# Optimization experiments

Hardware: AMD Instinct MI355X
Metric: run time of the kernel (lower is better)

The kernel has to match this reference:

```python
import jax, jax.numpy as jnp
import numpy as np

B, S, HID = 1, 2048, 2048
H, KVH, D = 16, 8, 128
QR, KR, VR = 6, 2, 2
SOFTCAP = 50.0
SCALING = D ** -0.5
NEG = -1e9


def _rope(Bfac, cos, sin):
    # Bfac: [b, s, r, d]; cos/sin: [s, d//2]; rotates adjacent pairs (complex view)
    x = Bfac.reshape(*Bfac.shape[:-1], D // 2, 2)
    xe, xo = x[..., 0], x[..., 1]
    c = cos[None, :, None, :]
    s = sin[None, :, None, :]
    oe = xe * c - xo * s
    oo = xe * s + xo * c
    return jnp.stack([oe, oo], axis=-1).reshape(Bfac.shape)


def setup_inputs() -> dict:
    key = jax.random.key(0)
    ks = jax.random.split(key, 12)
    hidden_states = jax.random.normal(ks[0], (B, S, HID), jnp.float32)
    # rotary tables (standard RoPE frequencies)
    inv_freq = 1.0 / (10000.0 ** (jnp.arange(0, D, 2, dtype=jnp.float32) / D))
    t = jnp.arange(S, dtype=jnp.float32)
    ang = t[:, None] * inv_freq[None, :]            # [S, D//2]
    cos, sin = jnp.cos(ang), jnp.sin(ang)
    # causal additive mask [1,1,S,S]
    causal = jnp.tril(jnp.ones((S, S), bool))
    mask = jnp.where(causal, 0.0, NEG).astype(jnp.float32)[None, None]
    kv_write_indices = jnp.arange(S, dtype=jnp.int32)
    sc = lambda k, shp: jax.random.normal(k, shp, jnp.float32) * (shp[0] ** -0.5)
    return {
        "hidden_states": hidden_states, "cos": cos, "sin": sin, "mask": mask,
        "kv_write_indices": kv_write_indices,
        "WAq": sc(ks[1], (HID, H * QR)), "WAk": sc(ks[2], (HID, KVH * KR)),
        "WAv": sc(ks[3], (HID, KVH * VR)), "WBq": sc(ks[4], (HID, QR * D)),
        "WBk": sc(ks[5], (HID, KR * D)), "WBv": sc(ks[6], (HID, VR * D)),
        "Wo": sc(ks[7], (H * D, HID)),
    }


def reference(hidden_states, cos, sin, mask, kv_write_indices,
              WAq, WAk, WAv, WBq, WBk, WBv, Wo):
    b, s, _ = hidden_states.shape
    # factor projections (never materialize full Q/K/V)
    A_q = (hidden_states @ WAq).reshape(b, s, H, QR)
    A_k = (hidden_states @ WAk).reshape(b, s, KVH, KR)
    A_v = (hidden_states @ WAv).reshape(b, s, KVH, VR)
    B_q = (hidden_states @ WBq).reshape(b, s, QR, D)
    B_k = (hidden_states @ WBk).reshape(b, s, KR, D)
    B_v = (hidden_states @ WBv).reshape(b, s, VR, D)
    # RoPE on B factors
    B_q = _rope(B_q, cos, sin)
    B_k = _rope(B_k, cos, sin)
    # prefill: kv_write_indices = arange(S) => cache slices equal current factors
    # GQA: broadcast KV heads up to H
    hpk = H // KVH
    A_k = jnp.repeat(A_k, hpk, axis=2)   # [b,k,H,KR]
    A_v = jnp.repeat(A_v, hpk, axis=2)   # [b,k,H,VR]
    # factor-expanded attention scores
    B_dots = jnp.einsum('bqrd,bksd->bqkrs', B_q, B_k) * SCALING
    attn = jnp.einsum('bqhr,bkhs,bqkrs->bhqk', A_q, A_k, B_dots)
    # logit softcapping
    attn = SOFTCAP * jnp.tanh(attn / SOFTCAP)
    attn = attn + mask
    probs = jax.nn.softmax(attn.astype(jnp.float32), axis=-1).astype(hidden_states.dtype)
    # factor-expanded output
    out = jnp.einsum('bhqk,bkhu,bkud->bhqd', probs, A_v, B_v)
    out = out.transpose(0, 2, 1, 3).reshape(b, s, H * D)
    return out @ Wo
```

## Files before the change

### kernel.cpp

```cpp
#include <hip/hip_runtime.h>


constexpr int SEQ   = 2048;
constexpr int HIDN  = 2048;
constexpr int NHEAD = 16;
constexpr int NKVH  = 8;
constexpr int DH    = 128;
constexpr int NCOLS = 1408;

typedef __bf16 bf16x8 __attribute__((ext_vector_type(8)));
typedef float  f32x4  __attribute__((ext_vector_type(4)));

#define MFMA(a, b, c) __builtin_amdgcn_mfma_f32_16x16x32_bf16((a), (b), (c), 0, 0, 0)

__device__ __forceinline__ void gload_lds16(const void* g, void* l) {
  __builtin_amdgcn_global_load_lds(
      (const __attribute__((address_space(1))) void*)g,
      (__attribute__((address_space(3))) void*)l, 16, 0, 0);
}


__global__ __launch_bounds__(256) void k_prep(
    const float* __restrict__ hidden,
    const float* __restrict__ WAq, const float* __restrict__ WAk,
    const float* __restrict__ WAv, const float* __restrict__ WBq,
    const float* __restrict__ WBk, const float* __restrict__ WBv,
    __bf16* __restrict__ hid_bf, __bf16* __restrict__ WT) {
  const int bid = blockIdx.x;
  if (bid < 2048) {
    const int i = (bid * 256 + threadIdx.x) * 8;
    f32x4 a = *(const f32x4*)(hidden + i);
    f32x4 b = *(const f32x4*)(hidden + i + 4);
    bf16x8 v;
#pragma unroll
    for (int j = 0; j < 4; j++) { v[j] = (__bf16)a[j]; v[4 + j] = (__bf16)b[j]; }
    *(bf16x8*)(hid_bf + i) = v;
  } else {
    const int t = bid - 2048;
    const int bc = (t % 44) * 32, bk = (t / 44) * 32;
    __shared__ float tl[32][33];
    const int tx = threadIdx.x & 31, ty = threadIdx.x >> 5;
    const int c = bc + tx;
#pragma unroll
    for (int j = 0; j < 32; j += 8) {
      const int k = bk + ty + j;
      float v;
      if (c < 96)        v = WAq[k * 96 + c];
      else if (c < 112)  v = WAk[k * 16 + (c - 96)];
      else if (c < 128)  v = WAv[k * 16 + (c - 112)];
      else if (c < 896)  v = WBq[k * 768 + (c - 128)];
      else if (c < 1152) v = WBk[k * 256 + (c - 896)];
      else               v = WBv[k * 256 + (c - 1152)];
      tl[ty + j][tx] = v;
    }
    __syncthreads();
#pragma unroll
    for (int j = 0; j < 32; j += 8)
      WT[(size_t)(bc + ty + j) * HIDN + bk + tx] = (__bf16)tl[tx][ty + j];
  }
}


__global__ __launch_bounds__(256) void k_proj_wo(
    const __bf16* __restrict__ A, const __bf16* __restrict__ BT,
    float* __restrict__ C0, float* __restrict__ C1,
    const float* __restrict__ Wo, __bf16* __restrict__ WoT) {
  __shared__ char smem[49152];
  const int bid = blockIdx.x;
  if (bid >= 704) {
    const int t = bid - 704;
    const int bn = (t % 64) * 32, bk = (t / 64) * 32;
    float (*tl)[33] = (float(*)[33])smem;
    const int tx = threadIdx.x & 31, ty = threadIdx.x >> 5;
#pragma unroll
    for (int j = 0; j < 32; j += 8)
      tl[ty + j][tx] = Wo[(size_t)(bk + ty + j) * HIDN + bn + tx];
    __syncthreads();
#pragma unroll
    for (int j = 0; j < 32; j += 8)
      WoT[(size_t)(bn + ty + j) * HIDN + bk + tx] = (__bf16)tl[tx][ty + j];
    return;
  }
  const int K = HIDN, N = NCOLS;
  __bf16* As = (__bf16*)smem;
  __bf16* Bs = (__bf16*)(smem + 32768);
  const int tid = threadIdx.x;
  const int w = tid >> 6, lane = tid & 63;
  const int lhi = lane >> 4, llo = lane & 15;
  const int wr = w >> 1, wc = w & 1;
  const int z = (bid >= 352);
  const int b = bid - z * 352;
  float* C = z ? C1 : C0;
  const int kbase = z * (K >> 1);
  const int sid = (b & 7) * 44 + (b >> 3);
  const int brow = (sid / 22) * 128, bcol = (sid % 22) * 64;
  const int rA = lane >> 2, kA = (lane & 3) * 8;
  const int nt = K >> 6;

  f32x4 acc[4][2];
#pragma unroll
  for (int m = 0; m < 4; m++)
#pragma unroll
    for (int n = 0; n < 2; n++) acc[m][n] = (f32x4){0.f, 0.f, 0.f, 0.f};

  auto stage = [&](int t) {
    const int buf = t & 3;
    const int k0 = kbase + t * 32;
#pragma unroll
    for (int i = 0; i < 2; i++) {
      int seg = w * 2 + i;
      int row = seg * 16 + rA;
      gload_lds16(A + (size_t)(brow + row) * K + k0 + kA,
                  As + buf * 4096 + seg * 512);
    }
    gload_lds16(BT + (size_t)(bcol + w * 16 + rA) * K + k0 + kA,
                Bs + buf * 2048 + w * 512);
  };

  stage(0); stage(1); stage(2);
  asm volatile("s_waitcnt vmcnt(6)" ::: "memory");
  __builtin_amdgcn_s_barrier();

  for (int t = 0; t < nt; t++) {
    if (t + 3 < nt) stage(t + 3);
    const int buf = t & 3;
    bf16x8 af[4], bfr[2];
#pragma unroll
    for (int m = 0; m < 4; m++)
      af[m] = *(const bf16x8*)&As[buf * 4096 + (wr * 64 + m * 16 + llo) * 32 + lhi * 8];
#pragma unroll
    for (int n = 0; n < 2; n++)
      bfr[n] = *(const bf16x8*)&Bs[buf * 2048 + (wc * 32 + n * 16 + llo) * 32 + lhi * 8];
#pragma unroll
    for (int m = 0; m < 4; m++)
#pragma unroll
      for (int n = 0; n < 2; n++) acc[m][n] = MFMA(af[m], bfr[n], acc[m][n]);
    const int rem = nt - 2 - t;
    if (rem >= 2)      asm volatile("s_waitcnt vmcnt(6)" ::: "memory");
    else if (rem == 1) asm volatile("s_waitcnt vmcnt(3)" ::: "memory");
    else               asm volatile("s_waitcnt vmcnt(0)" ::: "memory");
    __builtin_amdgcn_s_barrier();
  }

#pragma unroll
  for (int m = 0; m < 4; m++)
#pragma unroll
    for (int n = 0; n < 2; n++) {
      int r0 = brow + wr * 64 + m * 16 + lhi * 4;
      int c0 = bcol + wc * 32 + n * 16 + llo;
#pragma unroll
      for (int r = 0; r < 4; r++) C[(size_t)(r0 + r) * N + c0] = acc[m][n][r];
    }
}


__global__ __launch_bounds__(512) void k_gemm_out(const __bf16* __restrict__ A,
                                                  const __bf16* __restrict__ BT,
                                                  float* __restrict__ C) {
  __shared__ __bf16 As[3][8192];
  __shared__ __bf16 Bs[3][8192];
  const int K = HIDN, N = HIDN;
  const int tid = threadIdx.x;
  const int w = tid >> 6, lane = tid & 63;
  const int lhi = lane >> 4, llo = lane & 15;
  const int wr = w >> 2, wc = w & 3;

  const int id = blockIdx.y * 16 + blockIdx.x;
  const int g = id & 7, kk = id >> 3;
  const int rg = g >> 2, cg = g & 3;
  const int brow = (rg * 8 + (kk & 7)) * 128;
  const int bcol = (cg * 4 + (kk >> 3)) * 128;

  const int rA = tid >> 2, kA = (tid & 3) * 8;
  const int nt = K >> 6;

  f32x4 acc[4][2];
#pragma unroll
  for (int m = 0; m < 4; m++)
#pragma unroll
    for (int n = 0; n < 2; n++) acc[m][n] = (f32x4){0.f, 0.f, 0.f, 0.f};

  auto stage = [&](int t) {
    const int buf = t % 3;
    const int k0 = t * 64;
#pragma unroll
    for (int hf = 0; hf < 2; hf++) {
      gload_lds16(A  + (size_t)(brow + rA) * K + k0 + hf * 32 + kA,
                  &As[buf][hf * 4096 + w * 512]);
      gload_lds16(BT + (size_t)(bcol + rA) * K + k0 + hf * 32 + kA,
                  &Bs[buf][hf * 4096 + w * 512]);
    }
  };

  stage(0); stage(1);
  asm volatile("s_waitcnt vmcnt(4)" ::: "memory");
  __builtin_amdgcn_s_barrier();

  for (int t = 0; t < nt; t++) {
    if (t + 2 < nt) stage(t + 2);
    const int buf = t % 3;
#pragma unroll
    for (int hf = 0; hf < 2; hf++) {
      bf16x8 af[4], bfr[2];
#pragma unroll
      for (int m = 0; m < 4; m++)
        af[m] = *(const bf16x8*)&As[buf][hf * 4096 +
                                         (wr * 64 + m * 16 + llo) * 32 + lhi * 8];
#pragma unroll
      for (int n = 0; n < 2; n++)
        bfr[n] = *(const bf16x8*)&Bs[buf][hf * 4096 +
                                          (wc * 32 + n * 16 + llo) * 32 + lhi * 8];
#pragma unroll
      for (int m = 0; m < 4; m++)
#pragma unroll
        for (int n = 0; n < 2; n++) acc[m][n] = MFMA(af[m], bfr[n], acc[m][n]);
    }
    if (t + 2 < nt)      asm volatile("s_waitcnt vmcnt(4)" ::: "memory");
    else if (t + 1 < nt) asm volatile("s_waitcnt vmcnt(0)" ::: "memory");
    __builtin_amdgcn_s_barrier();
  }

#pragma unroll
  for (int m = 0; m < 4; m++)
#pragma unroll
    for (int n = 0; n < 2; n++) {
      int r0 = brow + wr * 64 + m * 16 + lhi * 4;
      int c0 = bcol + wc * 32 + n * 16 + llo;
#pragma unroll
      for (int r = 0; r < 4; r++) C[(size_t)(r0 + r) * N + c0] = acc[m][n][r];
    }
}


__global__ __launch_bounds__(128) void k_build_qkv(const float* __restrict__ P0,
                                                   const float* __restrict__ P1,
                                                   const float* __restrict__ cosT,
                                                   const float* __restrict__ sinT,
                                                   __bf16* __restrict__ Qo,
                                                   __bf16* __restrict__ Ko,
                                                   __bf16* __restrict__ Vto) {
  const int q = blockIdx.x, d = threadIdx.x;
  __shared__ float Ash[128];
  const float* r0 = P0 + (size_t)q * NCOLS;
  const float* r1 = P1 + (size_t)q * NCOLS;
  auto rd = [&](int i) { return r0[i] + r1[i]; };
  Ash[d] = rd(d);
  __syncthreads();
  const int m2 = (d >> 1) * 2;
  const bool odd = d & 1;
  const float c = cosT[q * 64 + (d >> 1)];
  const float s = sinT[q * 64 + (d >> 1)];

  float qacc[16];
#pragma unroll
  for (int h = 0; h < 16; h++) qacc[h] = 0.f;
#pragma unroll
  for (int r = 0; r < 6; r++) {
    float xe = rd(128 + r * 128 + m2);
    float xo = rd(128 + r * 128 + m2 + 1);
    float br = odd ? (xe * s + xo * c) : (xe * c - xo * s);
#pragma unroll
    for (int h = 0; h < 16; h++) qacc[h] += Ash[h * 6 + r] * br;
  }
#pragma unroll
  for (int h = 0; h < 16; h++)
    Qo[((size_t)h * SEQ + q) * DH + d] = (__bf16)(qacc[h] * 0.08838834764831845f);

  float kacc[8];
#pragma unroll
  for (int g = 0; g < 8; g++) kacc[g] = 0.f;
#pragma unroll
  for (int ss = 0; ss < 2; ss++) {
    float xe = rd(896 + ss * 128 + m2);
    float xo = rd(896 + ss * 128 + m2 + 1);
    float bs = odd ? (xe * s + xo * c) : (xe * c - xo * s);
#pragma unroll
    for (int g = 0; g < 8; g++) kacc[g] += Ash[96 + g * 2 + ss] * bs;
  }
#pragma unroll
  for (int g = 0; g < 8; g++)
    Ko[((size_t)g * SEQ + q) * DH + d] = (__bf16)kacc[g];

  float vacc[8];
#pragma unroll
  for (int g = 0; g < 8; g++) vacc[g] = 0.f;
#pragma unroll
  for (int u = 0; u < 2; u++) {
    float vu = rd(1152 + u * 128 + d);
#pragma unroll
    for (int g = 0; g < 8; g++) vacc[g] += Ash[112 + g * 2 + u] * vu;
  }
  const int qp = (q & ~31) | (((q & 15) >> 2) * 8 + (q & 3) + ((q & 16) >> 2));
#pragma unroll
  for (int g = 0; g < 8; g++)
    Vto[((size_t)g * DH + d) * SEQ + qp] = (__bf16)vacc[g];
}


__global__ __launch_bounds__(256) void k_attn(const __bf16* __restrict__ Q,
                                              const __bf16* __restrict__ Kc,
                                              const __bf16* __restrict__ Vt,
                                              float* __restrict__ AOf0,
                                              float* __restrict__ AOf1,
                                              float* __restrict__ Ls) {
  const int raw = blockIdx.x;
  const int g = raw & 7;
  const int j = raw >> 3;
  const int bqi = 31 - (j >> 2);
  const int hh = (j >> 1) & 1;
  const int p = j & 1;
  const int h = g * 2 + hh;
  const int w = threadIdx.x >> 6, lane = threadIdx.x & 63;
  const int lhi = lane >> 4, llo = lane & 15;
  const int q0 = bqi * 64 + w * 16;
  const int t0 = p * (bqi + 1), t1 = t0 + bqi + 1;

  __shared__ __bf16 KVs[2][8192];

  const __bf16* Qh = Q  + (size_t)h * SEQ * DH;
  const __bf16* Kg = Kc + (size_t)g * SEQ * DH;
  const __bf16* Vg = Vt + (size_t)g * DH * SEQ;
  float* AOc = p ? AOf1 : AOf0;

  bf16x8 aq[4];
#pragma unroll
  for (int c = 0; c < 4; c++)
    aq[c] = *(const bf16x8*)&Qh[(size_t)(q0 + llo) * DH + c * 32 + lhi * 8];

  f32x4 oacc[8];
  float lsum = 0.f;
#pragma unroll
  for (int n = 0; n < 8; n++) oacc[n] = (f32x4){0.f, 0.f, 0.f, 0.f};

  const int vb = llo * 64 + ((lhi ^ ((llo >> 1) & 3)) << 4);

  auto stage = [&](int kb, int buf) {
    __bf16* L = KVs[buf];
    if (w < 2) {
#pragma unroll
      for (int u = 0; u < 4; u++) {
        int c = w * 256 + u * 64 + lane;
        int row = c >> 4, jj = c & 15;
        gload_lds16(Kg + (size_t)(kb + row) * DH + ((jj ^ (row & 7)) * 8),
                    L + (w * 256 + u * 64) * 8);
      }
    } else {
#pragma unroll
      for (int u = 0; u < 4; u++) {
        int c = (w - 2) * 256 + u * 64 + lane;
        int d = c >> 2, jj = c & 3;
        gload_lds16(Vg + (size_t)d * SEQ + kb + ((jj ^ ((d >> 1) & 3)) * 8),
                    L + 4096 + ((w - 2) * 256 + u * 64) * 8);
      }
    }
  };

  stage(t0 * 32, t0 & 1);
  for (int t = t0; t < t1; t++) {
    const int kb = t * 32;
    const int buf = t & 1;
    if (t + 1 < t1) {
      stage(kb + 32, buf ^ 1);
      asm volatile("s_waitcnt vmcnt(4)" ::: "memory");
    } else {
      asm volatile("s_waitcnt vmcnt(0)" ::: "memory");
    }
    __builtin_amdgcn_s_barrier();
    if (kb <= q0 + 15) {
      const char* Kl = (const char*)KVs[buf];
      const char* Vl = (const char*)(KVs[buf] + 4096);
      f32x4 s0 = {0.f, 0.f, 0.f, 0.f}, s1 = {0.f, 0.f, 0.f, 0.f};
      __builtin_amdgcn_s_setprio(1);
#pragma unroll
      for (int c = 0; c < 4; c++) {
        const int row0 = llo, row1 = 16 + llo;
        bf16x8 k0 = *(const bf16x8*)(Kl + row0 * 256 +
                                     ((c * 64 + lhi * 16) ^ ((row0 & 7) << 4)));
        bf16x8 k1 = *(const bf16x8*)(Kl + row1 * 256 +
                                     ((c * 64 + lhi * 16) ^ ((row1 & 7) << 4)));
        s0 = MFMA(k0, aq[c], s0);
        s1 = MFMA(k1, aq[c], s1);
      }
      __builtin_amdgcn_s_setprio(0);
      float e[8];
#pragma unroll
      for (int r = 0; r < 4; r++) {
        float a0 = exp2f(s0[r] * 0.057707802f);
        float a1 = exp2f(s1[r] * 0.057707802f);
        e[r]     = exp2f(72.134752f - 144.269504f * __builtin_amdgcn_rcpf(a0 + 1.f));
        e[4 + r] = exp2f(72.134752f - 144.269504f * __builtin_amdgcn_rcpf(a1 + 1.f));
      }
      if (kb + 31 > q0) {
        const int qrow = q0 + llo;
#pragma unroll
        for (int r = 0; r < 4; r++) {
          if (kb + lhi * 4 + r > qrow)      e[r] = 0.f;
          if (kb + 16 + lhi * 4 + r > qrow) e[4 + r] = 0.f;
        }
      }
#pragma unroll
      for (int r = 0; r < 4; r++) lsum += e[r] + e[4 + r];
      union { bf16x8 v8; unsigned u[4]; } pu;
      asm("v_cvt_pk_bf16_f32 %0, %1, %2" : "=v"(pu.u[0]) : "v"(e[0]), "v"(e[1]));
      asm("v_cvt_pk_bf16_f32 %0, %1, %2" : "=v"(pu.u[1]) : "v"(e[2]), "v"(e[3]));
      asm("v_cvt_pk_bf16_f32 %0, %1, %2" : "=v"(pu.u[2]) : "v"(e[4]), "v"(e[5]));
      asm("v_cvt_pk_bf16_f32 %0, %1, %2" : "=v"(pu.u[3]) : "v"(e[6]), "v"(e[7]));
      __builtin_amdgcn_s_setprio(1);
#pragma unroll
      for (int n = 0; n < 8; n++) {
        bf16x8 vf = *(const bf16x8*)(Vl + vb + n * 1024);
        oacc[n] = MFMA(pu.v8, vf, oacc[n]);
      }
      __builtin_amdgcn_s_setprio(0);
    }
    asm volatile("" ::: "memory");
    __builtin_amdgcn_s_barrier();
  }

  float tsum = lsum;
  tsum += __shfl_xor(tsum, 16);
  tsum += __shfl_xor(tsum, 32);
  if (lhi == 0) Ls[((size_t)p * NHEAD + h) * SEQ + q0 + llo] = tsum;
#pragma unroll
  for (int r = 0; r < 4; r++) {
    const int qrow = q0 + lhi * 4 + r;
#pragma unroll
    for (int n = 0; n < 8; n++)
      AOc[(size_t)qrow * HIDN + h * DH + n * 16 + llo] = oacc[n][r];
  }
}


__global__ __launch_bounds__(256) void k_norm(const float* __restrict__ A0,
                                              const float* __restrict__ A1,
                                              const float* __restrict__ Ls,
                                              __bf16* __restrict__ AO) {
  const int i = (blockIdx.x * 256 + threadIdx.x) * 4;
  const int q = i >> 11, h = (i & 2047) >> 7;
  const float inv = 1.f / (Ls[h * SEQ + q] + Ls[(NHEAD + h) * SEQ + q]);
  f32x4 a = *(const f32x4*)(A0 + i);
  f32x4 b = *(const f32x4*)(A1 + i);
#pragma unroll
  for (int j = 0; j < 4; j++) AO[i + j] = (__bf16)((a[j] + b[j]) * inv);
}


extern "C" void kernel_launch(void* const* d_in, const int* in_sizes, int n_in,
                              void* d_out, int out_size, void* d_ws, size_t ws_size,
                              hipStream_t stream) {
  const float* hidden = (const float*)d_in[0];
  const float* cosT   = (const float*)d_in[1];
  const float* sinT   = (const float*)d_in[2];
  const float* WAq = (const float*)d_in[5];
  const float* WAk = (const float*)d_in[6];
  const float* WAv = (const float*)d_in[7];
  const float* WBq = (const float*)d_in[8];
  const float* WBk = (const float*)d_in[9];
  const float* WBv = (const float*)d_in[10];
  const float* Wo  = (const float*)d_in[11];
  float* out = (float*)d_out;

  char* ws = (char*)d_ws;
  __bf16* hid_bf = (__bf16*)(ws);
  __bf16* WallT  = (__bf16*)(ws + 8388608);
  float*  Pp0    = (float*)(ws + 14155776);
  __bf16* WoT    = (__bf16*)(ws + 25690112);
  __bf16* Qb     = (__bf16*)(ws + 34078720);
  __bf16* Kb     = (__bf16*)(ws + 42467328);
  __bf16* Vt     = (__bf16*)(ws + 46661632);
  float*  Pp1    = (float*)(ws + 50855936);
  float*  AOf0   = (float*)(ws);
  float*  AOf1   = (float*)(ws + 50855936);
  float*  Ls     = (float*)(ws + 67633152);
  __bf16* AO     = (__bf16*)(ws + 34078720);

  k_prep<<<2048 + 44 * 64, 256, 0, stream>>>(
      hidden, WAq, WAk, WAv, WBq, WBk, WBv, hid_bf, WallT);
  k_proj_wo<<<704 + 4096, 256, 0, stream>>>(hid_bf, WallT, Pp0, Pp1, Wo, WoT);
  k_build_qkv<<<SEQ, 128, 0, stream>>>(Pp0, Pp1, cosT, sinT, Qb, Kb, Vt);
  k_attn<<<1024, 256, 0, stream>>>(Qb, Kb, Vt, AOf0, AOf1, Ls);
  k_norm<<<(SEQ * HIDN / 4) / 256, 256, 0, stream>>>(AOf0, AOf1, Ls, AO);
  k_gemm_out<<<dim3(16, 16), 512, 0, stream>>>(AO, WoT, out);
}
```

Before: 141.5 us.

## Double the K-step per pipeline stage in projection GEMM with triple buffering

The projection GEMM now loads 64-wide K slices per stage, as two 32-wide halves, into a 3-deep LDS ring instead of 32-wide slices in a 4-deep ring. This halves the number of barrier/waitcnt iterations and doubles MFMA work per sync, raising LDS use to 72KB. Prefetch distance drops to 2 stages, which can expose more memory latency, and the higher LDS footprint may reduce blocks per CU.

```diff
diff --git a/kernel.cpp b/kernel.cpp
--- a/kernel.cpp
+++ b/kernel.cpp
@@ -65,7 +65,7 @@
     const __bf16* __restrict__ A, const __bf16* __restrict__ BT,
     float* __restrict__ C0, float* __restrict__ C1,
     const float* __restrict__ Wo, __bf16* __restrict__ WoT) {
-  __shared__ char smem[49152];
+  __shared__ char smem[73728];
   const int bid = blockIdx.x;
   if (bid >= 704) {
     const int t = bid - 704;
@@ -83,7 +83,7 @@
   }
   const int K = HIDN, N = NCOLS;
   __bf16* As = (__bf16*)smem;
-  __bf16* Bs = (__bf16*)(smem + 32768);
+  __bf16* Bs = (__bf16*)(smem + 49152);
   const int tid = threadIdx.x;
   const int w = tid >> 6, lane = tid & 63;
   const int lhi = lane >> 4, llo = lane & 15;
@@ -95,7 +95,7 @@
   const int sid = (b & 7) * 44 + (b >> 3);
   const int brow = (sid / 22) * 128, bcol = (sid % 22) * 64;
   const int rA = lane >> 2, kA = (lane & 3) * 8;
-  const int nt = K >> 6;
+  const int nt = K >> 7;
 
   f32x4 acc[4][2];
 #pragma unroll
@@ -104,41 +104,47 @@
     for (int n = 0; n < 2; n++) acc[m][n] = (f32x4){0.f, 0.f, 0.f, 0.f};
 
   auto stage = [&](int t) {
-    const int buf = t & 3;
-    const int k0 = kbase + t * 32;
-#pragma unroll
-    for (int i = 0; i < 2; i++) {
-      int seg = w * 2 + i;
-      int row = seg * 16 + rA;
-      gload_lds16(A + (size_t)(brow + row) * K + k0 + kA,
-                  As + buf * 4096 + seg * 512);
-    }
-    gload_lds16(BT + (size_t)(bcol + w * 16 + rA) * K + k0 + kA,
-                Bs + buf * 2048 + w * 512);
+    const int buf = t % 3;
+    const int k0 = kbase + t * 64;
+#pragma unroll
+    for (int hf = 0; hf < 2; hf++) {
+#pragma unroll
+      for (int i = 0; i < 2; i++) {
+        int seg = w * 2 + i;
+        int row = seg * 16 + rA;
+        gload_lds16(A + (size_t)(brow + row) * K + k0 + hf * 32 + kA,
+                    As + buf * 8192 + hf * 4096 + seg * 512);
+      }
+      gload_lds16(BT + (size_t)(bcol + w * 16 + rA) * K + k0 + hf * 32 + kA,
+                  Bs + buf * 4096 + hf * 2048 + w * 512);
+    }
   };
 
-  stage(0); stage(1); stage(2);
+  stage(0); stage(1);
   asm volatile("s_waitcnt vmcnt(6)" ::: "memory");
   __builtin_amdgcn_s_barrier();
 
   for (int t = 0; t < nt; t++) {
-    if (t + 3 < nt) stage(t + 3);
-    const int buf = t & 3;
-    bf16x8 af[4], bfr[2];
-#pragma unroll
-    for (int m = 0; m < 4; m++)
-      af[m] = *(const bf16x8*)&As[buf * 4096 + (wr * 64 + m * 16 + llo) * 32 + lhi * 8];
-#pragma unroll
-    for (int n = 0; n < 2; n++)
-      bfr[n] = *(const bf16x8*)&Bs[buf * 2048 + (wc * 32 + n * 16 + llo) * 32 + lhi * 8];
-#pragma unroll
-    for (int m = 0; m < 4; m++)
-#pragma unroll
-      for (int n = 0; n < 2; n++) acc[m][n] = MFMA(af[m], bfr[n], acc[m][n]);
-    const int rem = nt - 2 - t;
-    if (rem >= 2)      asm volatile("s_waitcnt vmcnt(6)" ::: "memory");
-    else if (rem == 1) asm volatile("s_waitcnt vmcnt(3)" ::: "memory");
-    else               asm volatile("s_waitcnt vmcnt(0)" ::: "memory");
+    if (t + 2 < nt) stage(t + 2);
+    const int buf = t % 3;
+#pragma unroll
+    for (int hf = 0; hf < 2; hf++) {
+      bf16x8 af[4], bfr[2];
+#pragma unroll
+      for (int m = 0; m < 4; m++)
+        af[m] = *(const bf16x8*)&As[buf * 8192 + hf * 4096 +
+                                    (wr * 64 + m * 16 + llo) * 32 + lhi * 8];
+#pragma unroll
+      for (int n = 0; n < 2; n++)
+        bfr[n] = *(const bf16x8*)&Bs[buf * 4096 + hf * 2048 +
+                                     (wc * 32 + n * 16 + llo) * 32 + lhi * 8];
+#pragma unroll
+      for (int m = 0; m < 4; m++)
+#pragma unroll
+        for (int n = 0; n < 2; n++) acc[m][n] = MFMA(af[m], bfr[n], acc[m][n]);
+    }
+    if (t + 2 < nt)      asm volatile("s_waitcnt vmcnt(6)" ::: "memory");
+    else if (t + 1 < nt) asm volatile("s_waitcnt vmcnt(0)" ::: "memory");
     __builtin_amdgcn_s_barrier();
   }
 
```

After: 141.3 us. Within noise of the previous version (-0.1%).
